# Optimization experiments

Measured on AMD Instinct MI355X. Metric: run time of the kernel, lower is better.

The kernel has to match this reference:

```python
import jax, jax.numpy as jnp
import numpy as np
from jax import lax

WINDOW_SIZE = 11
SIGMA = 1.5
RGB_RANGE = 1.0
K1, K2 = 0.01, 0.03
CHANNELS = 3


def gaussian_window(window_size, sigma, channels, dtype=jnp.float32):
    coords = jnp.arange(window_size, dtype=dtype) - window_size // 2
    g = jnp.exp(-(coords ** 2) / (2.0 * sigma * sigma))
    g = g / g.sum()
    w2d = jnp.outer(g, g)
    w2d = w2d / w2d.sum()
    # depthwise kernel: (C, 1, ws, ws) in OIHW with feature_group_count=C
    return jnp.broadcast_to(w2d, (channels, 1, window_size, window_size)).astype(dtype)


def _dwconv(inp, window, padding):
    # depthwise conv2d, groups = C
    C = inp.shape[1]
    return lax.conv_general_dilated(
        inp, window,
        window_strides=(1, 1),
        padding=[(padding, padding), (padding, padding)],
        feature_group_count=C,
        dimension_numbers=('NCHW', 'OIHW', 'NCHW'))


def setup_inputs() -> dict:
    key = jax.random.key(0)
    kx, ky = jax.random.split(key)
    B, C, H, W = 16, CHANNELS, 512, 512
    x = jax.random.uniform(kx, (B, C, H, W), dtype=jnp.float32)
    y = jax.random.uniform(ky, (B, C, H, W), dtype=jnp.float32)
    window = gaussian_window(WINDOW_SIZE, SIGMA, C)
    return {"x": x, "y": y, "window": window}


def reference(x, y, window):
    padding = WINDOW_SIZE // 2
    mu_x = _dwconv(x, window, padding)
    mu_y = _dwconv(y, window, padding)
    mu_x2 = mu_x * mu_x
    mu_y2 = mu_y * mu_y
    mu_xy = mu_x * mu_y
    sigma_x2 = _dwconv(x * x, window, padding) - mu_x2
    sigma_y2 = _dwconv(y * y, window, padding) - mu_y2
    sigma_xy = _dwconv(x * y, window, padding) - mu_xy
    L = RGB_RANGE
    C1 = (K1 * L) ** 2
    C2 = (K2 * L) ** 2
    ssim_map = ((2.0 * mu_xy + C1) * (2.0 * sigma_xy + C2)) / (
        (mu_x2 + mu_y2 + C1) * (sigma_x2 + sigma_y2 + C2) + 1e-12)
    loss = 1.0 - ssim_map
    return loss.mean()
```

## Files before the change

kernel.cpp:

```cpp
#include <hip/hip_runtime.h>


typedef __fp16 f16x8 __attribute__((ext_vector_type(8)));
typedef __fp16 f16x4 __attribute__((ext_vector_type(4)));
typedef float  f32x4 __attribute__((ext_vector_type(4)));
typedef unsigned u32x2 __attribute__((ext_vector_type(2)));
typedef unsigned u32x4 __attribute__((ext_vector_type(4)));

__device__ __forceinline__ unsigned pk2(float a, float b) {
    return __builtin_bit_cast(unsigned, __builtin_amdgcn_cvt_pkrtz(a, b));
}
__device__ __forceinline__ f32x4 mfmaB(f16x8 a, f16x8 b, f32x4 c) {
    return __builtin_amdgcn_mfma_f32_16x16x32_f16(a, b, c, 0, 0, 0);
}
__device__ __forceinline__ f32x4 mfmaC(f16x4 a, f16x4 b, f32x4 c) {
    return __builtin_amdgcn_mfma_f32_16x16x16f16(a, b, c, 0, 0, 0);
}
__device__ __forceinline__ void ldsBarrier() {
    asm volatile("s_waitcnt lgkmcnt(0)\n\ts_barrier" ::: "memory");
}

#define SXW 28

__global__ __launch_bounds__(256, 8) void ssim_main(
    const float* __restrict__ xg, const float* __restrict__ yg,
    const float* __restrict__ w2d, float* __restrict__ part)
{
    __shared__ __align__(16) unsigned sx[48 * SXW];
    __shared__ __align__(16) unsigned sy[48 * SXW];
    __shared__ unsigned tbp[64];
    __shared__ float gsf[11];
    __shared__ float wred[4];

    const int tid = threadIdx.x;

    const int nblk = (int)gridDim.x;
    const int bid = (int)blockIdx.x;
    const int swz = (bid & 7) * (nblk >> 3) + (bid >> 3);
    const int tz = swz >> 8, ty = (swz >> 4) & 15, tx = swz & 15;
    const int X0 = 32 * tx - 8, Y0 = 32 * ty - 8;
    const bool inter = (tx > 0) & (tx < 15) & (ty > 0) & (ty < 15);
    const float* __restrict__ xp = xg + (size_t)tz * (512 * 512);
    const float* __restrict__ yp = yg + (size_t)tz * (512 * 512);

    float4 lx0, ly0, lx1, ly1, lx2, ly2;
    const bool h2 = tid < 64;
    auto ldit = [&](int it, float4& vx, float4& vy) {
        const int r = it / 12, c4 = it - r * 12;
        const int gr = Y0 + r, gc0 = X0 + 4 * c4;
        if (inter) {
            const int o = gr * 512 + gc0;
            vx = *(const float4*)&xp[o];
            vy = *(const float4*)&yp[o];
        } else {
            const bool rok = (unsigned)gr < 512u;
            float tx4[4], ty4[4];
            #pragma unroll
            for (int j = 0; j < 4; ++j) {
                const int gc = gc0 + j;
                const bool ok = rok & ((unsigned)gc < 512u);
                const int o = ok ? (gr * 512 + gc) : 0;
                tx4[j] = ok ? xp[o] : 0.f;
                ty4[j] = ok ? yp[o] : 0.f;
            }
            vx = make_float4(tx4[0], tx4[1], tx4[2], tx4[3]);
            vy = make_float4(ty4[0], ty4[1], ty4[2], ty4[3]);
        }
    };
    ldit(tid, lx0, ly0);
    ldit(tid + 256, lx1, ly1);
    if (h2) ldit(tid + 512, lx2, ly2);

    if (tid < 11) {
        float s = 0.0f;
        #pragma unroll
        for (int j = 0; j < 11; ++j) s += w2d[tid * 11 + j];
        gsf[tid] = s;
    }
    if (tid < 64) {
        float ssum = 0.0f;
        #pragma unroll
        for (int k = 0; k < 11; ++k)
            if (k != 5) ssum += (float)(__fp16)gsf[k];
        const __fp16 cc = (__fp16)(1.0f - ssum);
        auto tap = [&](int t) -> __fp16 {
            if ((unsigned)t > 10u) return (__fp16)0.f;
            return (t == 5) ? cc : (__fp16)gsf[t];
        };
        const int t = tid - 19;
        const unsigned short lo = __builtin_bit_cast(unsigned short, tap(t));
        const unsigned short hi = __builtin_bit_cast(unsigned short, tap(t + 1));
        tbp[tid] = (unsigned)lo | ((unsigned)hi << 16);
    }

    auto wrt = [&](int it, const float4& vx, const float4& vy) {
        const int r = it / 12, c4 = it - r * 12;
        *(uint2*)&sx[r * SXW + 2 * c4] =
            make_uint2(pk2(vx.x, vx.y), pk2(vx.z, vx.w));
        *(uint2*)&sy[r * SXW + 2 * c4] =
            make_uint2(pk2(vy.x, vy.y), pk2(vy.z, vy.w));
    };
    wrt(tid, lx0, ly0);
    wrt(tid + 256, lx1, ly1);
    if (h2) wrt(tid + 512, lx2, ly2);
    ldsBarrier();

    const int lane = tid & 63, wv = tid >> 6;
    const int lm = lane & 15, lg = lane >> 4;
    const int wr = wv >> 1, wc = wv & 1;

    f16x8 bt;
    f16x4 ca0, ca1;
    {
        const int ib = 8 * lg - lm + 16;
        const u32x4 wb = {tbp[ib], tbp[ib + 2], tbp[ib + 4], tbp[ib + 6]};
        bt = __builtin_bit_cast(f16x8, wb);
        const int ic = 4 * lg - lm + 16;
        const u32x2 w0 = {tbp[ic], tbp[ic + 2]};
        const u32x2 w1 = {tbp[ic + 16], tbp[ic + 18]};
        ca0 = __builtin_bit_cast(f16x4, w0);
        ca1 = __builtin_bit_cast(f16x4, w1);
    }

    const int rbase = (16 * wr + lm) * SXW + 8 * wc + 4 * lg;
    const f16x8 xd0 = __builtin_bit_cast(f16x8, *(const u32x4*)&sx[rbase]);
    const f16x8 xd1 = __builtin_bit_cast(f16x8, *(const u32x4*)&sx[rbase + 16 * SXW]);
    const f16x8 yd0 = __builtin_bit_cast(f16x8, *(const u32x4*)&sy[rbase]);
    const f16x8 yd1 = __builtin_bit_cast(f16x8, *(const u32x4*)&sy[rbase + 16 * SXW]);

    const f32x4 z4 = {0.f, 0.f, 0.f, 0.f};
    f32x4 acc[5];
    #pragma unroll
    for (int q = 0; q < 5; ++q) {
        f16x8 a0, a1;
        if (q == 0)      { a0 = xd0;       a1 = xd1; }
        else if (q == 1) { a0 = yd0;       a1 = yd1; }
        else if (q == 2) { a0 = xd0 * xd0; a1 = xd1 * xd1; }
        else if (q == 3) { a0 = yd0 * yd0; a1 = yd1 * yd1; }
        else             { a0 = xd0 * yd0; a1 = xd1 * yd1; }
        const f32x4 d0 = mfmaB(a0, bt, z4);
        const f32x4 d1 = mfmaB(a1, bt, z4);
        const u32x2 h0 = {pk2(d0[0], d0[1]), pk2(d0[2], d0[3])};
        const u32x2 h1 = {pk2(d1[0], d1[1]), pk2(d1[2], d1[3])};
        const f32x4 p0 = mfmaC(ca0, __builtin_bit_cast(f16x4, h0), z4);
        acc[q]         = mfmaC(ca1, __builtin_bit_cast(f16x4, h1), p0);
    }

    float lsum = 0.0f;
    const float C1 = 1e-4f, C2 = 9e-4f;
    #pragma unroll
    for (int r = 0; r < 4; ++r) {
        const float mx = acc[0][r], my = acc[1][r];
        const float exx = acc[2][r], eyy = acc[3][r];
        const float exy = acc[4][r];
        const float mx2 = mx * mx, my2 = my * my, mxy = mx * my;
        const float vx = exx - mx2, vy = eyy - my2, vxy = exy - mxy;
        const float num = (2.0f * mxy + C1) * (2.0f * vxy + C2);
        const float den = (mx2 + my2 + C1) * (vx + vy + C2) + 1e-12f;
        lsum = fmaf(num, __builtin_amdgcn_rcpf(den), lsum);
    }

    #pragma unroll
    for (int off = 32; off > 0; off >>= 1)
        lsum += __shfl_down(lsum, off, 64);
    if ((tid & 63) == 0) wred[tid >> 6] = lsum;
    ldsBarrier();
    if (tid == 0)
        part[bid] = wred[0] + wred[1] + wred[2] + wred[3];
}

__global__ __launch_bounds__(1024) void ssim_reduce(
    const float* __restrict__ part, float* __restrict__ out,
    int n, float invN)
{
    __shared__ float wred[16];
    float s = 0.0f;
    for (int i = threadIdx.x; i < n; i += 1024) s += part[i];
    #pragma unroll
    for (int off = 32; off > 0; off >>= 1)
        s += __shfl_down(s, off, 64);
    if ((threadIdx.x & 63) == 0) wred[threadIdx.x >> 6] = s;
    __syncthreads();
    if (threadIdx.x == 0) {
        float tot = 0.0f;
        #pragma unroll
        for (int w = 0; w < 16; ++w) tot += wred[w];
        out[0] = 1.0f - tot * invN;
    }
}

extern "C" void kernel_launch(void* const* d_in, const int* in_sizes, int n_in,
                              void* d_out, int out_size, void* d_ws, size_t ws_size,
                              hipStream_t stream) {
    const float* x   = (const float*)d_in[0];
    const float* y   = (const float*)d_in[1];
    const float* w2d = (const float*)d_in[2];
    float* out  = (float*)d_out;
    float* part = (float*)d_ws;

    const int H = 512, W = 512;
    const int total = in_sizes[0];
    const int Z = total / (H * W);

    const int nblk = Z * 256;
    ssim_main<<<dim3(nblk), 256, 0, stream>>>(x, y, w2d, part);

    const float invN = 1.0f / (float)total;
    ssim_reduce<<<1, 1024, 0, stream>>>(part, out, nblk, invN);
}
```

Measured before the change: 142.3 us.

## Process eight tiles per block with double-buffered LDS prefetch

Each block now loops over eight consecutive 32x32 tiles instead of one. It loads the next tile's global data into registers while computing the current tile from a double-buffered LDS stage. The aim is to hide global load latency and to amortise per-block setup (the Gaussian tap table and the reduction). The cost is fewer blocks, a lower occupancy hint (launch bounds 8 to 6), more LDS, a barrier per tile, and added register pressure from the prefetch values held across the compute.

```diff
diff --git a/kernel.cpp b/kernel.cpp
--- a/kernel.cpp
+++ b/kernel.cpp
@@ -21,55 +21,71 @@
 }
 
 #define SXW 28
-
-__global__ __launch_bounds__(256, 8) void ssim_main(
+#define TPB 8
+
+__global__ __launch_bounds__(256, 6) void ssim_main(
     const float* __restrict__ xg, const float* __restrict__ yg,
     const float* __restrict__ w2d, float* __restrict__ part)
 {
-    __shared__ __align__(16) unsigned sx[48 * SXW];
-    __shared__ __align__(16) unsigned sy[48 * SXW];
+    __shared__ __align__(16) unsigned sx[2][48 * SXW];
+    __shared__ __align__(16) unsigned sy[2][48 * SXW];
     __shared__ unsigned tbp[64];
     __shared__ float gsf[11];
     __shared__ float wred[4];
 
     const int tid = threadIdx.x;
-
     const int nblk = (int)gridDim.x;
     const int bid = (int)blockIdx.x;
-    const int swz = (bid & 7) * (nblk >> 3) + (bid >> 3);
-    const int tz = swz >> 8, ty = (swz >> 4) & 15, tx = swz & 15;
-    const int X0 = 32 * tx - 8, Y0 = 32 * ty - 8;
-    const bool inter = (tx > 0) & (tx < 15) & (ty > 0) & (ty < 15);
-    const float* __restrict__ xp = xg + (size_t)tz * (512 * 512);
-    const float* __restrict__ yp = yg + (size_t)tz * (512 * 512);
+    const int swzb = (bid & 7) * (nblk >> 3) + (bid >> 3);
+    const int tbase = swzb * TPB;
 
     float4 lx0, ly0, lx1, ly1, lx2, ly2;
     const bool h2 = tid < 64;
-    auto ldit = [&](int it, float4& vx, float4& vy) {
-        const int r = it / 12, c4 = it - r * 12;
-        const int gr = Y0 + r, gc0 = X0 + 4 * c4;
-        if (inter) {
-            const int o = gr * 512 + gc0;
-            vx = *(const float4*)&xp[o];
-            vy = *(const float4*)&yp[o];
-        } else {
-            const bool rok = (unsigned)gr < 512u;
-            float tx4[4], ty4[4];
-            #pragma unroll
-            for (int j = 0; j < 4; ++j) {
-                const int gc = gc0 + j;
-                const bool ok = rok & ((unsigned)gc < 512u);
-                const int o = ok ? (gr * 512 + gc) : 0;
-                tx4[j] = ok ? xp[o] : 0.f;
-                ty4[j] = ok ? yp[o] : 0.f;
+    auto ldtile = [&](int i) {
+        const int t = tbase + i;
+        const int tz = t >> 8, ty = (t >> 4) & 15, tx = t & 15;
+        const int X0 = 32 * tx - 8, Y0 = 32 * ty - 8;
+        const bool inter = (tx > 0) & (tx < 15) & (ty > 0) & (ty < 15);
+        const float* __restrict__ xp = xg + (size_t)tz * (512 * 512);
+        const float* __restrict__ yp = yg + (size_t)tz * (512 * 512);
+        auto ldit = [&](int it, float4& vx, float4& vy) {
+            const int r = it / 12, c4 = it - r * 12;
+            const int gr = Y0 + r, gc0 = X0 + 4 * c4;
+            if (inter) {
+                const int o = gr * 512 + gc0;
+                vx = *(const float4*)&xp[o];
+                vy = *(const float4*)&yp[o];
+            } else {
+                const bool rok = (unsigned)gr < 512u;
+                float tx4[4], ty4[4];
+                #pragma unroll
+                for (int j = 0; j < 4; ++j) {
+                    const int gc = gc0 + j;
+                    const bool ok = rok & ((unsigned)gc < 512u);
+                    const int o = ok ? (gr * 512 + gc) : 0;
+                    tx4[j] = ok ? xp[o] : 0.f;
+                    ty4[j] = ok ? yp[o] : 0.f;
+                }
+                vx = make_float4(tx4[0], tx4[1], tx4[2], tx4[3]);
+                vy = make_float4(ty4[0], ty4[1], ty4[2], ty4[3]);
             }
-            vx = make_float4(tx4[0], tx4[1], tx4[2], tx4[3]);
-            vy = make_float4(ty4[0], ty4[1], ty4[2], ty4[3]);
-        }
+        };
+        ldit(tid, lx0, ly0);
+        ldit(tid + 256, lx1, ly1);
+        if (h2) ldit(tid + 512, lx2, ly2);
     };
-    ldit(tid, lx0, ly0);
-    ldit(tid + 256, lx1, ly1);
-    if (h2) ldit(tid + 512, lx2, ly2);
+    auto stage = [&](int buf) {
+        auto wrt = [&](int it, const float4& vx, const float4& vy) {
+            const int r = it / 12, c4 = it - r * 12;
+            *(uint2*)&sx[buf][r * SXW + 2 * c4] =
+                make_uint2(pk2(vx.x, vx.y), pk2(vx.z, vx.w));
+            *(uint2*)&sy[buf][r * SXW + 2 * c4] =
+                make_uint2(pk2(vy.x, vy.y), pk2(vy.z, vy.w));
+        };
+        wrt(tid, lx0, ly0);
+        wrt(tid + 256, lx1, ly1);
+        if (h2) wrt(tid + 512, lx2, ly2);
+    };
 
     if (tid < 11) {
         float s = 0.0f;
@@ -93,16 +109,8 @@
         tbp[tid] = (unsigned)lo | ((unsigned)hi << 16);
     }
 
-    auto wrt = [&](int it, const float4& vx, const float4& vy) {
-        const int r = it / 12, c4 = it - r * 12;
-        *(uint2*)&sx[r * SXW + 2 * c4] =
-            make_uint2(pk2(vx.x, vx.y), pk2(vx.z, vx.w));
-        *(uint2*)&sy[r * SXW + 2 * c4] =
-            make_uint2(pk2(vy.x, vy.y), pk2(vy.z, vy.w));
-    };
-    wrt(tid, lx0, ly0);
-    wrt(tid + 256, lx1, ly1);
-    if (h2) wrt(tid + 512, lx2, ly2);
+    ldtile(0);
+    stage(0);
     ldsBarrier();
 
     const int lane = tid & 63, wv = tid >> 6;
@@ -123,41 +131,52 @@
     }
 
     const int rbase = (16 * wr + lm) * SXW + 8 * wc + 4 * lg;
-    const f16x8 xd0 = __builtin_bit_cast(f16x8, *(const u32x4*)&sx[rbase]);
-    const f16x8 xd1 = __builtin_bit_cast(f16x8, *(const u32x4*)&sx[rbase + 16 * SXW]);
-    const f16x8 yd0 = __builtin_bit_cast(f16x8, *(const u32x4*)&sy[rbase]);
-    const f16x8 yd1 = __builtin_bit_cast(f16x8, *(const u32x4*)&sy[rbase + 16 * SXW]);
-
     const f32x4 z4 = {0.f, 0.f, 0.f, 0.f};
-    f32x4 acc[5];
-    #pragma unroll
-    for (int q = 0; q < 5; ++q) {
-        f16x8 a0, a1;
-        if (q == 0)      { a0 = xd0;       a1 = xd1; }
-        else if (q == 1) { a0 = yd0;       a1 = yd1; }
-        else if (q == 2) { a0 = xd0 * xd0; a1 = xd1 * xd1; }
-        else if (q == 3) { a0 = yd0 * yd0; a1 = yd1 * yd1; }
-        else             { a0 = xd0 * yd0; a1 = xd1 * yd1; }
-        const f32x4 d0 = mfmaB(a0, bt, z4);
-        const f32x4 d1 = mfmaB(a1, bt, z4);
-        const u32x2 h0 = {pk2(d0[0], d0[1]), pk2(d0[2], d0[3])};
-        const u32x2 h1 = {pk2(d1[0], d1[1]), pk2(d1[2], d1[3])};
-        const f32x4 p0 = mfmaC(ca0, __builtin_bit_cast(f16x4, h0), z4);
-        acc[q]         = mfmaC(ca1, __builtin_bit_cast(f16x4, h1), p0);
-    }
-
+    const float C1 = 1e-4f, C2 = 9e-4f;
     float lsum = 0.0f;
-    const float C1 = 1e-4f, C2 = 9e-4f;
-    #pragma unroll
-    for (int r = 0; r < 4; ++r) {
-        const float mx = acc[0][r], my = acc[1][r];
-        const float exx = acc[2][r], eyy = acc[3][r];
-        const float exy = acc[4][r];
-        const float mx2 = mx * mx, my2 = my * my, mxy = mx * my;
-        const float vx = exx - mx2, vy = eyy - my2, vxy = exy - mxy;
-        const float num = (2.0f * mxy + C1) * (2.0f * vxy + C2);
-        const float den = (mx2 + my2 + C1) * (vx + vy + C2) + 1e-12f;
-        lsum = fmaf(num, __builtin_amdgcn_rcpf(den), lsum);
+
+    for (int i = 0; i < TPB; ++i) {
+        const int cur = i & 1;
+        if (i + 1 < TPB) ldtile(i + 1);
+
+        const unsigned* __restrict__ sxc = sx[cur];
+        const unsigned* __restrict__ syc = sy[cur];
+        const f16x8 xd0 = __builtin_bit_cast(f16x8, *(const u32x4*)&sxc[rbase]);
+        const f16x8 xd1 = __builtin_bit_cast(f16x8, *(const u32x4*)&sxc[rbase + 16 * SXW]);
+        const f16x8 yd0 = __builtin_bit_cast(f16x8, *(const u32x4*)&syc[rbase]);
+        const f16x8 yd1 = __builtin_bit_cast(f16x8, *(const u32x4*)&syc[rbase + 16 * SXW]);
+
+        f32x4 acc[5];
+        #pragma unroll
+        for (int q = 0; q < 5; ++q) {
+            f16x8 a0, a1;
+            if (q == 0)      { a0 = xd0;       a1 = xd1; }
+            else if (q == 1) { a0 = yd0;       a1 = yd1; }
+            else if (q == 2) { a0 = xd0 * xd0; a1 = xd1 * xd1; }
+            else if (q == 3) { a0 = yd0 * yd0; a1 = yd1 * yd1; }
+            else             { a0 = xd0 * yd0; a1 = xd1 * yd1; }
+            const f32x4 d0 = mfmaB(a0, bt, z4);
+            const f32x4 d1 = mfmaB(a1, bt, z4);
+            const u32x2 h0 = {pk2(d0[0], d0[1]), pk2(d0[2], d0[3])};
+            const u32x2 h1 = {pk2(d1[0], d1[1]), pk2(d1[2], d1[3])};
+            const f32x4 p0 = mfmaC(ca0, __builtin_bit_cast(f16x4, h0), z4);
+            acc[q]         = mfmaC(ca1, __builtin_bit_cast(f16x4, h1), p0);
+        }
+
+        #pragma unroll
+        for (int r = 0; r < 4; ++r) {
+            const float mx = acc[0][r], my = acc[1][r];
+            const float exx = acc[2][r], eyy = acc[3][r];
+            const float exy = acc[4][r];
+            const float mx2 = mx * mx, my2 = my * my, mxy = mx * my;
+            const float vx = exx - mx2, vy = eyy - my2, vxy = exy - mxy;
+            const float num = (2.0f * mxy + C1) * (2.0f * vxy + C2);
+            const float den = (mx2 + my2 + C1) * (vx + vy + C2) + 1e-12f;
+            lsum = fmaf(num, __builtin_amdgcn_rcpf(den), lsum);
+        }
+
+        if (i + 1 < TPB) stage(cur ^ 1);
+        ldsBarrier();
     }
 
     #pragma unroll
@@ -202,7 +221,7 @@
     const int total = in_sizes[0];
     const int Z = total / (H * W);
 
-    const int nblk = Z * 256;
+    const int nblk = Z * 256 / TPB;
     ssim_main<<<dim3(nblk), 256, 0, stream>>>(x, y, w2d, part);
 
     const float invN = 1.0f / (float)total;
```

Result: slower. 214.8 us (+50.9%).
